# Optimization experiments

Measured on AMD Instinct MI355X. Metric: run time of the kernel, lower is better.

## Reference

```python
import jax, jax.numpy as jnp
import numpy as np

B, S, D = 2, 256, 768
NUM_SPANS = 3
PROJ_DIM = 128


def _span_indices(seq_len):
    # (i, j) pairs exactly as the original double loop enumerates them;
    # span_idx fills slots 0..N-1 of the zero-initialized buffer sequentially.
    si, ei = [], []
    for i in range(seq_len):
        for j in range(i, min(seq_len, i + NUM_SPANS)):
            si.append(i)
            ei.append(j)
    return np.asarray(si, np.int32), np.asarray(ei, np.int32)


def setup_inputs() -> dict:
    key = jax.random.key(0)
    ks = jax.random.split(key, 6)
    sc = 0.02
    return {
        "hidden": jax.random.normal(ks[0], (B, S, D), jnp.float32),
        "width_emb": jax.random.normal(ks[1], (NUM_SPANS, D), jnp.float32) * sc,
        "w_span": jax.random.normal(ks[2], (3 * D, D), jnp.float32) * sc,
        "b_span": jnp.zeros((D,), jnp.float32),
        "w_cls": jax.random.normal(ks[3], (D, 1), jnp.float32) * sc,
        "b_cls": jnp.zeros((1,), jnp.float32),
        "w_p1": jax.random.normal(ks[4], (D, D), jnp.float32) * sc,
        "b_p1": jnp.zeros((D,), jnp.float32),
        "w_p2": jax.random.normal(ks[5], (D, PROJ_DIM), jnp.float32) * sc,
        "b_p2": jnp.zeros((PROJ_DIM,), jnp.float32),
    }


def reference(hidden, width_emb, w_span, b_span, w_cls, b_cls, w_p1, b_p1, w_p2, b_p2):
    Bv, Sv, Dv = hidden.shape
    total = Sv * (Sv + 1) // 2  # size of the zero-padded span buffer
    si, ei = _span_indices(Sv)
    n_valid = si.shape[0]  # 3*S - 3 actually-filled spans

    start = hidden[:, si]                      # [B, N, D] fused gather
    end = hidden[:, ei]                        # [B, N, D]
    w = width_emb[ei - si]                     # [N, D] width-embed lookup
    valid = jnp.concatenate(
        [start, end, jnp.broadcast_to(w[None], (Bv, n_valid, Dv))], axis=-1
    )  # [B, N, 3D]
    pad = jnp.zeros((Bv, total - n_valid, 3 * Dv), hidden.dtype)
    span_vecs = jnp.concatenate([valid, pad], axis=1)  # [B, total, 3D]

    span = span_vecs @ w_span + b_span          # span_rep: [B, total, D]
    logits = (span @ w_cls + b_cls)[..., 0]     # classifier: [B, total]
    proj = jax.nn.relu(span @ w_p1 + b_p1) @ w_p2 + b_p2  # [B, total, 128]
    return logits, proj
```

## Files before the change

kernel.cpp:

```cpp
#include <hip/hip_runtime.h>


typedef unsigned short u16;
typedef __attribute__((ext_vector_type(8))) short bf16x8;
typedef __attribute__((ext_vector_type(8))) unsigned short u16x8;
typedef __attribute__((ext_vector_type(4))) float f32x4;

#define D 768
#define S 256
#define TOTAL 32896
#define NVALID 765
#define NPADROW (TOTAL - NVALID)
#define PD 128
#define LOGITS_SZ (2 * TOTAL)
#define MROWS 1088

#define WS_P1   0
#define WS_TPAD 835584
#define WS_L    836352
#define WS_LW   837376
#define WS_LPAD 837379
#define WS_PPAD 837380
#define US_BYTE_OFF (837632 * 4)
#define US_HH  0
#define US_HL  835584
#define US_AH  1671168
#define US_AL  2064384
#define US_B1H 2457600
#define US_B1L 3637248
#define US_W1H 4816896
#define US_W1L 5406720

__device__ __forceinline__ u16 f2bf(float v) {
    unsigned u = __float_as_uint(v);
    u += 0x7fffu + ((u >> 16) & 1u);
    return (u16)(u >> 16);
}
__device__ __forceinline__ float bf2f(u16 h) {
    return __uint_as_float(((unsigned)h) << 16);
}

__device__ __forceinline__ void span_iw(int k, int& i, int& w) {
    if (k < 762)      { i = k / 3;  w = k - i * 3; }
    else if (k < 764) { i = 254;    w = k - 762; }
    else              { i = 255;    w = 0; }
}

__global__ __launch_bounds__(256) void k_prep(const float* __restrict__ hidden,
                                              const float* __restrict__ width_emb,
                                              const float* __restrict__ w_span,
                                              const float* __restrict__ b_span,
                                              const float* __restrict__ w_cls,
                                              const float* __restrict__ b_cls,
                                              const float* __restrict__ w_p1,
                                              const float* __restrict__ b_p1,
                                              float* __restrict__ ws) {
    u16* us = (u16*)((char*)ws + US_BYTE_OFF);
    const int bid = blockIdx.x, tid = threadIdx.x;
    __shared__ u16 Th[64][72];
    __shared__ u16 Tl[64][72];
    __shared__ float red[256];

    if (bid < 192) {
        const int e0 = bid * 2048 + tid * 8;
        float4 v0 = *(const float4*)&hidden[e0];
        float4 v1 = *(const float4*)&hidden[e0 + 4];
        float f[8] = {v0.x, v0.y, v0.z, v0.w, v1.x, v1.y, v1.z, v1.w};
        u16x8 h, l;
        #pragma unroll
        for (int c = 0; c < 8; ++c) {
            u16 hh = f2bf(f[c]);
            h[c] = hh;
            l[c] = f2bf(f[c] - bf2f(hh));
        }
        *(u16x8*)&us[US_AH + e0] = h;
        *(u16x8*)&us[US_AL + e0] = l;
        return;
    }
    const float* tsrc = nullptr;
    u16 *tdh = nullptr, *tdl = nullptr;
    int kb = 0, nb = 0;
    if (bid < 480) {
        int t2 = bid - 192;
        int g = t2 / 144, rem = t2 % 144;
        kb = rem / 12; nb = rem % 12;
        tsrc = w_span + (size_t)g * D * D;
        tdh = us + US_B1H + (size_t)g * D * D;
        tdl = us + US_B1L + (size_t)g * D * D;
    } else if (bid < 624) {
        int t3 = bid - 480;
        kb = t3 / 12; nb = t3 % 12;
        tsrc = w_p1;
        tdh = us + US_W1H;
        tdl = us + US_W1L;
    }
    if (tsrc) {
        #pragma unroll
        for (int r4 = 0; r4 < 4; ++r4) {
            const int srow = r4 * 16 + (tid >> 4);
            const int scol = (tid & 15) * 4;
            float4 v = *(const float4*)&tsrc[(size_t)(kb * 64 + srow) * D + nb * 64 + scol];
            float f[4] = {v.x, v.y, v.z, v.w};
            #pragma unroll
            for (int c = 0; c < 4; ++c) {
                u16 hh = f2bf(f[c]);
                Th[scol + c][srow] = hh;
                Tl[scol + c][srow] = f2bf(f[c] - bf2f(hh));
            }
        }
        __syncthreads();
        const int orow = tid >> 2, kp = (tid & 3) * 16;
        const size_t didx = (size_t)(nb * 64 + orow) * D + kb * 64 + kp;
        *(u16x8*)&tdh[didx]     = *(const u16x8*)&Th[orow][kp];
        *(u16x8*)&tdh[didx + 8] = *(const u16x8*)&Th[orow][kp + 8];
        *(u16x8*)&tdl[didx]     = *(const u16x8*)&Tl[orow][kp];
        *(u16x8*)&tdl[didx + 8] = *(const u16x8*)&Tl[orow][kp + 8];
        return;
    }
    const int dl = tid & 63, kc = tid >> 6;
    if (bid < 660) {
        const int t4 = bid - 624;
        const int w = t4 / 12, seg = t4 % 12;
        const int d = seg * 64 + dl;
        const float* Aw = w_span + (size_t)(2 * D) * D;
        const float* we = width_emb + w * D;
        float p = 0.f;
        #pragma unroll 4
        for (int k = kc * 192; k < kc * 192 + 192; ++k)
            p = fmaf(we[k], Aw[(size_t)k * D + d], p);
        red[tid] = p; __syncthreads();
        if (kc == 0) {
            float v = red[dl] + red[64 + dl] + red[128 + dl] + red[192 + dl] + b_span[d];
            u16 hh = f2bf(v);
            const size_t idx = (size_t)(1024 + w) * D + d;
            us[US_HH + idx] = hh;
            us[US_HL + idx] = f2bf(v - bf2f(hh));
        }
    } else if (bid < 672) {
        const int d = (bid - 660) * 64 + dl;
        float p = 0.f;
        #pragma unroll 4
        for (int k = kc * 192; k < kc * 192 + 192; ++k)
            p = fmaf(b_span[k], w_p1[(size_t)k * D + d], p);
        red[tid] = p; __syncthreads();
        if (kc == 0) {
            float v = red[dl] + red[64 + dl] + red[128 + dl] + red[192 + dl] + b_p1[d];
            ws[WS_TPAD + d] = fmaxf(v, 0.f);
        }
    } else {
        if (tid < 64) {
            float a = 0.f;
            #pragma unroll
            for (int i = 0; i < 12; ++i) a = fmaf(b_span[tid + 64 * i], w_cls[tid + 64 * i], a);
            for (int off = 32; off > 0; off >>= 1) a += __shfl_down(a, off, 64);
            if (tid == 0) ws[WS_LPAD] = a + b_cls[0];
        }
    }
}

#define MFMA(A, B, C) __builtin_amdgcn_mfma_f32_16x16x32_bf16(A, B, C, 0, 0, 0)

__global__ __launch_bounds__(256) void k_mg1(const float* __restrict__ w_p2,
                                             const float* __restrict__ b_p2,
                                             float* __restrict__ ws) {
    u16* us = (u16*)((char*)ws + US_BYTE_OFF);
    const int bid = blockIdx.x, tid = threadIdx.x;
    __shared__ u16 LA_h[64][40], LA_l[64][40], LB_h[64][40], LB_l[64][40];
    __shared__ float redp[128];
    if (bid < 192) {
        const int mt = bid / 24, nt = bid % 24;
        const int m0 = mt * 64, n0 = nt * 64;
        const int row = tid >> 2, kp = (tid & 3) * 8;
        const u16* Ah = us + US_AH; const u16* Al = us + US_AL;
        const u16* Bh = us + US_B1H; const u16* Bl = us + US_B1L;
        const size_t aoff = (size_t)(m0 + row) * D + kp;
        const size_t boff = (size_t)(n0 + row) * D + kp;
        u16x8 ra_h = *(const u16x8*)&Ah[aoff];
        u16x8 ra_l = *(const u16x8*)&Al[aoff];
        u16x8 rb_h = *(const u16x8*)&Bh[boff];
        u16x8 rb_l = *(const u16x8*)&Bl[boff];
        const int wv = tid >> 6, lane = tid & 63;
        const int wm = wv & 1, wn = wv >> 1;
        const int lr = lane & 15, lk = (lane >> 4) * 8;
        f32x4 acc00 = {0,0,0,0}, acc01 = {0,0,0,0}, acc10 = {0,0,0,0}, acc11 = {0,0,0,0};
        for (int kt = 0; kt < 24; ++kt) {
            *(u16x8*)&LA_h[row][kp] = ra_h;
            *(u16x8*)&LA_l[row][kp] = ra_l;
            *(u16x8*)&LB_h[row][kp] = rb_h;
            *(u16x8*)&LB_l[row][kp] = rb_l;
            __syncthreads();
            if (kt < 23) {
                ra_h = *(const u16x8*)&Ah[aoff + (kt + 1) * 32];
                ra_l = *(const u16x8*)&Al[aoff + (kt + 1) * 32];
                rb_h = *(const u16x8*)&Bh[boff + (kt + 1) * 32];
                rb_l = *(const u16x8*)&Bl[boff + (kt + 1) * 32];
            }
            bf16x8 ah0 = *(const bf16x8*)&LA_h[wm * 32 + lr][lk];
            bf16x8 ah1 = *(const bf16x8*)&LA_h[wm * 32 + 16 + lr][lk];
            bf16x8 al0 = *(const bf16x8*)&LA_l[wm * 32 + lr][lk];
            bf16x8 al1 = *(const bf16x8*)&LA_l[wm * 32 + 16 + lr][lk];
            bf16x8 bh0 = *(const bf16x8*)&LB_h[wn * 32 + lr][lk];
            bf16x8 bh1 = *(const bf16x8*)&LB_h[wn * 32 + 16 + lr][lk];
            bf16x8 bl0 = *(const bf16x8*)&LB_l[wn * 32 + lr][lk];
            bf16x8 bl1 = *(const bf16x8*)&LB_l[wn * 32 + 16 + lr][lk];
            acc00 = MFMA(ah0, bh0, acc00); acc00 = MFMA(ah0, bl0, acc00); acc00 = MFMA(al0, bh0, acc00);
            acc01 = MFMA(ah0, bh1, acc01); acc01 = MFMA(ah0, bl1, acc01); acc01 = MFMA(al0, bh1, acc01);
            acc10 = MFMA(ah1, bh0, acc10); acc10 = MFMA(ah1, bl0, acc10); acc10 = MFMA(al1, bh0, acc10);
            acc11 = MFMA(ah1, bh1, acc11); acc11 = MFMA(ah1, bl1, acc11); acc11 = MFMA(al1, bh1, acc11);
            __syncthreads();
        }
        const int g = (n0 >= D);
        u16* Hh = us + US_HH; u16* Hl = us + US_HL;
        #define WR1(ACC, FM, FN) { \
            const int rr0 = g * 512 + m0 + wm * 32 + FM * 16 + (lane >> 4) * 4; \
            const int cc = n0 - g * D + wn * 32 + FN * 16 + lr; \
            _Pragma("unroll") \
            for (int r = 0; r < 4; ++r) { \
                float v = ACC[r]; \
                u16 hh = f2bf(v); \
                const size_t idx = (size_t)(rr0 + r) * D + cc; \
                Hh[idx] = hh; Hl[idx] = f2bf(v - bf2f(hh)); \
            } }
        WR1(acc00, 0, 0) WR1(acc01, 0, 1) WR1(acc10, 1, 0) WR1(acc11, 1, 1)
        #undef WR1
    } else {
        const int j = tid & 127, h2 = tid >> 7;
        float acc = 0.f;
        #pragma unroll 4
        for (int it = 0; it < 384; ++it) {
            const int d = h2 * 384 + it;
            acc = fmaf(ws[WS_TPAD + d], w_p2[(size_t)d * PD + j], acc);
        }
        if (h2) redp[j] = acc;
        __syncthreads();
        if (!h2) ws[WS_PPAD + j] = acc + redp[j] + b_p2[j];
    }
}

__global__ __launch_bounds__(256) void k_mg2(const float* __restrict__ w_cls,
                                             const float* __restrict__ b_cls,
                                             float* __restrict__ ws) {
    u16* us = (u16*)((char*)ws + US_BYTE_OFF);
    const int bid = blockIdx.x, tid = threadIdx.x;
    __shared__ u16 LA_h[64][40], LA_l[64][40], LB_h[64][40], LB_l[64][40];
    if (bid < 204) {
        const int mt = bid / 12, nt = bid % 12;
        const int m0 = mt * 64, n0 = nt * 64;
        const int row = tid >> 2, kp = (tid & 3) * 8;
        const u16* Ah = us + US_HH; const u16* Al = us + US_HL;
        const u16* Bh = us + US_W1H; const u16* Bl = us + US_W1L;
        const size_t aoff = (size_t)(m0 + row) * D + kp;
        const size_t boff = (size_t)(n0 + row) * D + kp;
        u16x8 ra_h = *(const u16x8*)&Ah[aoff];
        u16x8 ra_l = *(const u16x8*)&Al[aoff];
        u16x8 rb_h = *(const u16x8*)&Bh[boff];
        u16x8 rb_l = *(const u16x8*)&Bl[boff];
        const int wv = tid >> 6, lane = tid & 63;
        const int wm = wv & 1, wn = wv >> 1;
        const int lr = lane & 15, lk = (lane >> 4) * 8;
        f32x4 acc00 = {0,0,0,0}, acc01 = {0,0,0,0}, acc10 = {0,0,0,0}, acc11 = {0,0,0,0};
        for (int kt = 0; kt < 24; ++kt) {
            *(u16x8*)&LA_h[row][kp] = ra_h;
            *(u16x8*)&LA_l[row][kp] = ra_l;
            *(u16x8*)&LB_h[row][kp] = rb_h;
            *(u16x8*)&LB_l[row][kp] = rb_l;
            __syncthreads();
            if (kt < 23) {
                ra_h = *(const u16x8*)&Ah[aoff + (kt + 1) * 32];
                ra_l = *(const u16x8*)&Al[aoff + (kt + 1) * 32];
                rb_h = *(const u16x8*)&Bh[boff + (kt + 1) * 32];
                rb_l = *(const u16x8*)&Bl[boff + (kt + 1) * 32];
            }
            bf16x8 ah0 = *(const bf16x8*)&LA_h[wm * 32 + lr][lk];
            bf16x8 ah1 = *(const bf16x8*)&LA_h[wm * 32 + 16 + lr][lk];
            bf16x8 al0 = *(const bf16x8*)&LA_l[wm * 32 + lr][lk];
            bf16x8 al1 = *(const bf16x8*)&LA_l[wm * 32 + 16 + lr][lk];
            bf16x8 bh0 = *(const bf16x8*)&LB_h[wn * 32 + lr][lk];
            bf16x8 bh1 = *(const bf16x8*)&LB_h[wn * 32 + 16 + lr][lk];
            bf16x8 bl0 = *(const bf16x8*)&LB_l[wn * 32 + lr][lk];
            bf16x8 bl1 = *(const bf16x8*)&LB_l[wn * 32 + 16 + lr][lk];
            acc00 = MFMA(ah0, bh0, acc00); acc00 = MFMA(ah0, bl0, acc00); acc00 = MFMA(al0, bh0, acc00);
            acc01 = MFMA(ah0, bh1, acc01); acc01 = MFMA(ah0, bl1, acc01); acc01 = MFMA(al0, bh1, acc01);
            acc10 = MFMA(ah1, bh0, acc10); acc10 = MFMA(ah1, bl0, acc10); acc10 = MFMA(al1, bh0, acc10);
            acc11 = MFMA(ah1, bh1, acc11); acc11 = MFMA(ah1, bl1, acc11); acc11 = MFMA(al1, bh1, acc11);
            __syncthreads();
        }
        float* P1 = ws + WS_P1;
        #define WR2(ACC, FM, FN) { \
            const int rr0 = m0 + wm * 32 + FM * 16 + (lane >> 4) * 4; \
            const int cc = n0 + wn * 32 + FN * 16 + lr; \
            _Pragma("unroll") \
            for (int r = 0; r < 4; ++r) \
                P1[(size_t)(rr0 + r) * D + cc] = ACC[r]; \
            }
        WR2(acc00, 0, 0) WR2(acc01, 0, 1) WR2(acc10, 1, 0) WR2(acc11, 1, 1)
        #undef WR2
    } else if (bid < 236) {
        const int w64 = tid >> 6, lane = tid & 63;
        const int rbase = (bid - 204) * 32 + w64 * 8;
        for (int rr = 0; rr < 8; ++rr) {
            const int r = rbase + rr;
            const u16* hh = us + US_HH + (size_t)r * D;
            const u16* hl = us + US_HL + (size_t)r * D;
            float a = 0.f;
            #pragma unroll
            for (int i = 0; i < 12; ++i) {
                const int d = lane + 64 * i;
                a = fmaf(bf2f(hh[d]) + bf2f(hl[d]), w_cls[d], a);
            }
            for (int off = 32; off > 0; off >>= 1) a += __shfl_down(a, off, 64);
            if (lane == 0) ws[WS_L + r] = a;
        }
    } else {
        if (tid < 192) {
            const int w = tid >> 6, lane = tid & 63;
            const u16* hh = us + US_HH + (size_t)(1024 + w) * D;
            const u16* hl = us + US_HL + (size_t)(1024 + w) * D;
            float a = 0.f;
            #pragma unroll
            for (int i = 0; i < 12; ++i) {
                const int d = lane + 64 * i;
                a = fmaf(bf2f(hh[d]) + bf2f(hl[d]), w_cls[d], a);
            }
            for (int off = 32; off > 0; off >>= 1) a += __shfl_down(a, off, 64);
            if (lane == 0) ws[WS_LW + w] = a + b_cls[0];
        }
    }
}

__global__ __launch_bounds__(256) void k_stage3(const float* __restrict__ w_p2,
                                                const float* __restrict__ b_p1,
                                                const float* __restrict__ b_p2,
                                                const float* __restrict__ ws,
                                                float* __restrict__ out) {
    const int bid = blockIdx.x, tid = threadIdx.x;
    if (bid < 512) {
        const int t0 = bid * 256 + tid;
        if (t0 < 2 * NPADROW) {
            int b = t0 / NPADROW;
            out[b * TOTAL + NVALID + (t0 - b * NPADROW)] = ws[WS_LPAD];
        }
        const float4 pp = *(const float4*)&ws[WS_PPAD + ((tid & 31) << 2)];
        float4* out4 = (float4*)(out + LOGITS_SZ);
        const long long totalU = (long long)2 * NPADROW * 32;
        for (long long u = t0; u < totalU; u += 131072) {
            int rb = (int)(u >> 5);
            int b = rb / NPADROW;
            int kk = rb - b * NPADROW;
            out4[((size_t)b * TOTAL + NVALID + kk) * 32 + (int)(u & 31)] = pp;
        }
        return;
    }
    const int sb = bid - 512;
    __shared__ float tld[D * 5];
    __shared__ float red[4 * PD];
    const float* P1 = ws + WS_P1;
    {
        const int s = tid >> 6, dl = tid & 63;
        const int q = sb * 4 + s;
        const int v = q < 1530;
        const int qc = v ? q : 0;
        const int b = qc >= 765;
        const int k = qc - 765 * b;
        int i, w; span_iw(k, i, w);
        const size_t rs = (size_t)(b * S + i) * D;
        const size_t re = (size_t)(512 + b * S + i + w) * D;
        const size_t rw = (size_t)(1024 + w) * D;
        #pragma unroll
        for (int p = 0; p < 12; ++p) {
            const int dd = dl + 64 * p;
            float val = P1[rs + dd] + P1[re + dd] + P1[rw + dd] + b_p1[dd];
            tld[dd * 5 + s] = v ? fmaxf(val, 0.f) : 0.f;
        }
    }
    if (tid < 4) {
        int q2 = sb * 4 + tid;
        if (q2 < 1530) {
            int b2 = q2 >= 765, k2 = q2 - 765 * b2, i2, w2;
            span_iw(k2, i2, w2);
            out[b2 * TOTAL + k2] = ws[WS_L + b2 * S + i2]
                                 + ws[WS_L + 512 + b2 * S + i2 + w2] + ws[WS_LW + w2];
        }
    }
    __syncthreads();
    const int j = tid & 127, h = tid >> 7;
    float a[4] = {0.f, 0.f, 0.f, 0.f};
    const float* wp = w_p2 + (size_t)h * 384 * PD + j;
    const float* tb = tld + h * 384 * 5;
    #pragma unroll 4
    for (int it = 0; it < 384; ++it) {
        float wv = wp[(size_t)it * PD];
        #pragma unroll
        for (int s4 = 0; s4 < 4; ++s4)
            a[s4] = fmaf(wv, tb[it * 5 + s4], a[s4]);
    }
    if (h) {
        #pragma unroll
        for (int s4 = 0; s4 < 4; ++s4) red[s4 * PD + j] = a[s4];
    }
    __syncthreads();
    if (!h) {
        const float bp = b_p2[j];
        #pragma unroll
        for (int s4 = 0; s4 < 4; ++s4) {
            int q2 = sb * 4 + s4;
            if (q2 < 1530) {
                int b2 = q2 >= 765, k2 = q2 - 765 * b2;
                out[LOGITS_SZ + ((size_t)b2 * TOTAL + k2) * PD + j] =
                    a[s4] + red[s4 * PD + j] + bp;
            }
        }
    }
}

extern "C" void kernel_launch(void* const* d_in, const int* in_sizes, int n_in,
                              void* d_out, int out_size, void* d_ws, size_t ws_size,
                              hipStream_t stream) {
    const float* hidden    = (const float*)d_in[0];
    const float* width_emb = (const float*)d_in[1];
    const float* w_span    = (const float*)d_in[2];
    const float* b_span    = (const float*)d_in[3];
    const float* w_cls     = (const float*)d_in[4];
    const float* b_cls     = (const float*)d_in[5];
    const float* w_p1      = (const float*)d_in[6];
    const float* b_p1      = (const float*)d_in[7];
    const float* w_p2      = (const float*)d_in[8];
    const float* b_p2      = (const float*)d_in[9];
    float* out = (float*)d_out;
    float* ws  = (float*)d_ws;

    k_prep<<<673, 256, 0, stream>>>(hidden, width_emb, w_span, b_span, w_cls, b_cls,
                                    w_p1, b_p1, ws);
    k_mg1<<<193, 256, 0, stream>>>(w_p2, b_p2, ws);
    k_mg2<<<237, 256, 0, stream>>>(w_cls, b_cls, ws);
    k_stage3<<<895, 256, 0, stream>>>(w_p2, b_p1, b_p2, ws, out);
}
```

Before: 182.7 us.

## Use per-wave LDS-free MFMA tiles and finer span blocks for more parallelism

Both split-bf16 GEMMs drop their 64x64 block tiles that were staged through shared memory and synchronised every k-step. Each wave now loads its own 16x32 tile operands straight from global memory into registers, which gives many more waves and no barriers. The pad-row projection is moved from the first GEMM kernel into the second. The stage-3 kernel now handles 2 spans per block instead of 4, so it launches more blocks. The cost is more redundant global or L2 traffic because tiles are no longer shared through LDS, and each block in stage 3 reuses w_p2 less.

```diff
diff --git a/kernel.cpp b/kernel.cpp
--- a/kernel.cpp
+++ b/kernel.cpp
@@ -159,149 +159,105 @@
 }
 
 #define MFMA(A, B, C) __builtin_amdgcn_mfma_f32_16x16x32_bf16(A, B, C, 0, 0, 0)
-
-__global__ __launch_bounds__(256) void k_mg1(const float* __restrict__ w_p2,
-                                             const float* __restrict__ b_p2,
-                                             float* __restrict__ ws) {
+#define LD8(P) (*(const bf16x8*)(P))
+
+__global__ __launch_bounds__(256) void k_g1(float* __restrict__ ws) {
+    u16* us = (u16*)((char*)ws + US_BYTE_OFF);
+    const int wid = blockIdx.x * 4 + (threadIdx.x >> 6);
+    const int lane = threadIdx.x & 63;
+    const int mt = wid & 31, nt = wid >> 5;
+    const int m0 = mt * 16, n0 = nt * 32;
+    const int lr = lane & 15, lk8 = (lane >> 4) * 8;
+    const u16* Ah = us + US_AH; const u16* Al = us + US_AL;
+    const u16* Bh = us + US_B1H; const u16* Bl = us + US_B1L;
+    const size_t aoff = (size_t)(m0 + lr) * D + lk8;
+    const size_t b0 = (size_t)(n0 + lr) * D + lk8;
+    const size_t b1 = b0 + (size_t)16 * D;
+    f32x4 acc0 = {0,0,0,0}, acc1 = {0,0,0,0};
+    bf16x8 ah = LD8(Ah + aoff), al = LD8(Al + aoff);
+    bf16x8 bh0 = LD8(Bh + b0), bl0 = LD8(Bl + b0);
+    bf16x8 bh1 = LD8(Bh + b1), bl1 = LD8(Bl + b1);
+    for (int kt = 0; kt < 24; ++kt) {
+        bf16x8 cah = ah, cal = al, cbh0 = bh0, cbl0 = bl0, cbh1 = bh1, cbl1 = bl1;
+        if (kt < 23) {
+            const size_t o = (size_t)(kt + 1) * 32;
+            ah = LD8(Ah + aoff + o); al = LD8(Al + aoff + o);
+            bh0 = LD8(Bh + b0 + o);  bl0 = LD8(Bl + b0 + o);
+            bh1 = LD8(Bh + b1 + o);  bl1 = LD8(Bl + b1 + o);
+        }
+        acc0 = MFMA(cah, cbh0, acc0);
+        acc0 = MFMA(cah, cbl0, acc0);
+        acc0 = MFMA(cal, cbh0, acc0);
+        acc1 = MFMA(cah, cbh1, acc1);
+        acc1 = MFMA(cah, cbl1, acc1);
+        acc1 = MFMA(cal, cbh1, acc1);
+    }
+    const int g = (n0 >= D);
+    const int cb = n0 - g * D;
+    const int row0 = g * 512 + m0 + (lane >> 4) * 4;
+    u16* Hh = us + US_HH; u16* Hl = us + US_HL;
+    #pragma unroll
+    for (int r = 0; r < 4; ++r) {
+        const size_t base = (size_t)(row0 + r) * D;
+        float v0 = acc0[r], v1 = acc1[r];
+        u16 h0 = f2bf(v0), h1 = f2bf(v1);
+        Hh[base + cb + lr] = h0;       Hl[base + cb + lr] = f2bf(v0 - bf2f(h0));
+        Hh[base + cb + 16 + lr] = h1;  Hl[base + cb + 16 + lr] = f2bf(v1 - bf2f(h1));
+    }
+}
+
+__global__ __launch_bounds__(256) void k_g2(const float* __restrict__ w_cls,
+                                            const float* __restrict__ b_cls,
+                                            const float* __restrict__ w_p2,
+                                            const float* __restrict__ b_p2,
+                                            float* __restrict__ ws) {
     u16* us = (u16*)((char*)ws + US_BYTE_OFF);
     const int bid = blockIdx.x, tid = threadIdx.x;
-    __shared__ u16 LA_h[64][40], LA_l[64][40], LB_h[64][40], LB_l[64][40];
-    __shared__ float redp[128];
-    if (bid < 192) {
-        const int mt = bid / 24, nt = bid % 24;
-        const int m0 = mt * 64, n0 = nt * 64;
-        const int row = tid >> 2, kp = (tid & 3) * 8;
-        const u16* Ah = us + US_AH; const u16* Al = us + US_AL;
-        const u16* Bh = us + US_B1H; const u16* Bl = us + US_B1L;
-        const size_t aoff = (size_t)(m0 + row) * D + kp;
-        const size_t boff = (size_t)(n0 + row) * D + kp;
-        u16x8 ra_h = *(const u16x8*)&Ah[aoff];
-        u16x8 ra_l = *(const u16x8*)&Al[aoff];
-        u16x8 rb_h = *(const u16x8*)&Bh[boff];
-        u16x8 rb_l = *(const u16x8*)&Bl[boff];
-        const int wv = tid >> 6, lane = tid & 63;
-        const int wm = wv & 1, wn = wv >> 1;
-        const int lr = lane & 15, lk = (lane >> 4) * 8;
-        f32x4 acc00 = {0,0,0,0}, acc01 = {0,0,0,0}, acc10 = {0,0,0,0}, acc11 = {0,0,0,0};
+    const u16* Hh = us + US_HH; const u16* Hl = us + US_HL;
+    if (bid < 390) {
+        const int wid = bid * 4 + (tid >> 6);
+        const int lane = tid & 63;
+        const int mt = wid % 65, nt = wid / 65;
+        const int m0 = mt * 16, n0 = nt * 32;
+        const int lr = lane & 15, lk8 = (lane >> 4) * 8;
+        const u16* Bh = us + US_W1H; const u16* Bl = us + US_W1L;
+        const size_t aoff = (size_t)(m0 + lr) * D + lk8;
+        const size_t b0 = (size_t)(n0 + lr) * D + lk8;
+        const size_t b1 = b0 + (size_t)16 * D;
+        f32x4 acc0 = {0,0,0,0}, acc1 = {0,0,0,0};
+        bf16x8 ah = LD8(Hh + aoff), al = LD8(Hl + aoff);
+        bf16x8 bh0 = LD8(Bh + b0), bl0 = LD8(Bl + b0);
+        bf16x8 bh1 = LD8(Bh + b1), bl1 = LD8(Bl + b1);
         for (int kt = 0; kt < 24; ++kt) {
-            *(u16x8*)&LA_h[row][kp] = ra_h;
-            *(u16x8*)&LA_l[row][kp] = ra_l;
-            *(u16x8*)&LB_h[row][kp] = rb_h;
-            *(u16x8*)&LB_l[row][kp] = rb_l;
-            __syncthreads();
+            bf16x8 cah = ah, cal = al, cbh0 = bh0, cbl0 = bl0, cbh1 = bh1, cbl1 = bl1;
             if (kt < 23) {
-                ra_h = *(const u16x8*)&Ah[aoff + (kt + 1) * 32];
-                ra_l = *(const u16x8*)&Al[aoff + (kt + 1) * 32];
-                rb_h = *(const u16x8*)&Bh[boff + (kt + 1) * 32];
-                rb_l = *(const u16x8*)&Bl[boff + (kt + 1) * 32];
+                const size_t o = (size_t)(kt + 1) * 32;
+                ah = LD8(Hh + aoff + o); al = LD8(Hl + aoff + o);
+                bh0 = LD8(Bh + b0 + o);  bl0 = LD8(Bl + b0 + o);
+                bh1 = LD8(Bh + b1 + o);  bl1 = LD8(Bl + b1 + o);
             }
-            bf16x8 ah0 = *(const bf16x8*)&LA_h[wm * 32 + lr][lk];
-            bf16x8 ah1 = *(const bf16x8*)&LA_h[wm * 32 + 16 + lr][lk];
-            bf16x8 al0 = *(const bf16x8*)&LA_l[wm * 32 + lr][lk];
-            bf16x8 al1 = *(const bf16x8*)&LA_l[wm * 32 + 16 + lr][lk];
-            bf16x8 bh0 = *(const bf16x8*)&LB_h[wn * 32 + lr][lk];
-            bf16x8 bh1 = *(const bf16x8*)&LB_h[wn * 32 + 16 + lr][lk];
-            bf16x8 bl0 = *(const bf16x8*)&LB_l[wn * 32 + lr][lk];
-            bf16x8 bl1 = *(const bf16x8*)&LB_l[wn * 32 + 16 + lr][lk];
-            acc00 = MFMA(ah0, bh0, acc00); acc00 = MFMA(ah0, bl0, acc00); acc00 = MFMA(al0, bh0, acc00);
-            acc01 = MFMA(ah0, bh1, acc01); acc01 = MFMA(ah0, bl1, acc01); acc01 = MFMA(al0, bh1, acc01);
-            acc10 = MFMA(ah1, bh0, acc10); acc10 = MFMA(ah1, bl0, acc10); acc10 = MFMA(al1, bh0, acc10);
-            acc11 = MFMA(ah1, bh1, acc11); acc11 = MFMA(ah1, bl1, acc11); acc11 = MFMA(al1, bh1, acc11);
-            __syncthreads();
-        }
-        const int g = (n0 >= D);
-        u16* Hh = us + US_HH; u16* Hl = us + US_HL;
-        #define WR1(ACC, FM, FN) { \
-            const int rr0 = g * 512 + m0 + wm * 32 + FM * 16 + (lane >> 4) * 4; \
-            const int cc = n0 - g * D + wn * 32 + FN * 16 + lr; \
-            _Pragma("unroll") \
-            for (int r = 0; r < 4; ++r) { \
-                float v = ACC[r]; \
-                u16 hh = f2bf(v); \
-                const size_t idx = (size_t)(rr0 + r) * D + cc; \
-                Hh[idx] = hh; Hl[idx] = f2bf(v - bf2f(hh)); \
-            } }
-        WR1(acc00, 0, 0) WR1(acc01, 0, 1) WR1(acc10, 1, 0) WR1(acc11, 1, 1)
-        #undef WR1
-    } else {
-        const int j = tid & 127, h2 = tid >> 7;
-        float acc = 0.f;
-        #pragma unroll 4
-        for (int it = 0; it < 384; ++it) {
-            const int d = h2 * 384 + it;
-            acc = fmaf(ws[WS_TPAD + d], w_p2[(size_t)d * PD + j], acc);
-        }
-        if (h2) redp[j] = acc;
-        __syncthreads();
-        if (!h2) ws[WS_PPAD + j] = acc + redp[j] + b_p2[j];
-    }
-}
-
-__global__ __launch_bounds__(256) void k_mg2(const float* __restrict__ w_cls,
-                                             const float* __restrict__ b_cls,
-                                             float* __restrict__ ws) {
-    u16* us = (u16*)((char*)ws + US_BYTE_OFF);
-    const int bid = blockIdx.x, tid = threadIdx.x;
-    __shared__ u16 LA_h[64][40], LA_l[64][40], LB_h[64][40], LB_l[64][40];
-    if (bid < 204) {
-        const int mt = bid / 12, nt = bid % 12;
-        const int m0 = mt * 64, n0 = nt * 64;
-        const int row = tid >> 2, kp = (tid & 3) * 8;
-        const u16* Ah = us + US_HH; const u16* Al = us + US_HL;
-        const u16* Bh = us + US_W1H; const u16* Bl = us + US_W1L;
-        const size_t aoff = (size_t)(m0 + row) * D + kp;
-        const size_t boff = (size_t)(n0 + row) * D + kp;
-        u16x8 ra_h = *(const u16x8*)&Ah[aoff];
-        u16x8 ra_l = *(const u16x8*)&Al[aoff];
-        u16x8 rb_h = *(const u16x8*)&Bh[boff];
-        u16x8 rb_l = *(const u16x8*)&Bl[boff];
-        const int wv = tid >> 6, lane = tid & 63;
-        const int wm = wv & 1, wn = wv >> 1;
-        const int lr = lane & 15, lk = (lane >> 4) * 8;
-        f32x4 acc00 = {0,0,0,0}, acc01 = {0,0,0,0}, acc10 = {0,0,0,0}, acc11 = {0,0,0,0};
-        for (int kt = 0; kt < 24; ++kt) {
-            *(u16x8*)&LA_h[row][kp] = ra_h;
-            *(u16x8*)&LA_l[row][kp] = ra_l;
-            *(u16x8*)&LB_h[row][kp] = rb_h;
-            *(u16x8*)&LB_l[row][kp] = rb_l;
-            __syncthreads();
-            if (kt < 23) {
-                ra_h = *(const u16x8*)&Ah[aoff + (kt + 1) * 32];
-                ra_l = *(const u16x8*)&Al[aoff + (kt + 1) * 32];
-                rb_h = *(const u16x8*)&Bh[boff + (kt + 1) * 32];
-                rb_l = *(const u16x8*)&Bl[boff + (kt + 1) * 32];
-            }
-            bf16x8 ah0 = *(const bf16x8*)&LA_h[wm * 32 + lr][lk];
-            bf16x8 ah1 = *(const bf16x8*)&LA_h[wm * 32 + 16 + lr][lk];
-            bf16x8 al0 = *(const bf16x8*)&LA_l[wm * 32 + lr][lk];
-            bf16x8 al1 = *(const bf16x8*)&LA_l[wm * 32 + 16 + lr][lk];
-            bf16x8 bh0 = *(const bf16x8*)&LB_h[wn * 32 + lr][lk];
-            bf16x8 bh1 = *(const bf16x8*)&LB_h[wn * 32 + 16 + lr][lk];
-            bf16x8 bl0 = *(const bf16x8*)&LB_l[wn * 32 + lr][lk];
-            bf16x8 bl1 = *(const bf16x8*)&LB_l[wn * 32 + 16 + lr][lk];
-            acc00 = MFMA(ah0, bh0, acc00); acc00 = MFMA(ah0, bl0, acc00); acc00 = MFMA(al0, bh0, acc00);
-            acc01 = MFMA(ah0, bh1, acc01); acc01 = MFMA(ah0, bl1, acc01); acc01 = MFMA(al0, bh1, acc01);
-            acc10 = MFMA(ah1, bh0, acc10); acc10 = MFMA(ah1, bl0, acc10); acc10 = MFMA(al1, bh0, acc10);
-            acc11 = MFMA(ah1, bh1, acc11); acc11 = MFMA(ah1, bl1, acc11); acc11 = MFMA(al1, bh1, acc11);
-            __syncthreads();
+            acc0 = MFMA(cah, cbh0, acc0);
+            acc0 = MFMA(cah, cbl0, acc0);
+            acc0 = MFMA(cal, cbh0, acc0);
+            acc1 = MFMA(cah, cbh1, acc1);
+            acc1 = MFMA(cah, cbl1, acc1);
+            acc1 = MFMA(cal, cbh1, acc1);
         }
         float* P1 = ws + WS_P1;
-        #define WR2(ACC, FM, FN) { \
-            const int rr0 = m0 + wm * 32 + FM * 16 + (lane >> 4) * 4; \
-            const int cc = n0 + wn * 32 + FN * 16 + lr; \
-            _Pragma("unroll") \
-            for (int r = 0; r < 4; ++r) \
-                P1[(size_t)(rr0 + r) * D + cc] = ACC[r]; \
-            }
-        WR2(acc00, 0, 0) WR2(acc01, 0, 1) WR2(acc10, 1, 0) WR2(acc11, 1, 1)
-        #undef WR2
-    } else if (bid < 236) {
+        const int row0 = m0 + (lane >> 4) * 4;
+        #pragma unroll
+        for (int r = 0; r < 4; ++r) {
+            const size_t base = (size_t)(row0 + r) * D;
+            P1[base + n0 + lr] = acc0[r];
+            P1[base + n0 + 16 + lr] = acc1[r];
+        }
+    } else if (bid < 422) {
         const int w64 = tid >> 6, lane = tid & 63;
-        const int rbase = (bid - 204) * 32 + w64 * 8;
+        const int rbase = (bid - 390) * 32 + w64 * 8;
         for (int rr = 0; rr < 8; ++rr) {
             const int r = rbase + rr;
-            const u16* hh = us + US_HH + (size_t)r * D;
-            const u16* hl = us + US_HL + (size_t)r * D;
+            const u16* hh = Hh + (size_t)r * D;
+            const u16* hl = Hl + (size_t)r * D;
             float a = 0.f;
             #pragma unroll
             for (int i = 0; i < 12; ++i) {
@@ -311,11 +267,11 @@
             for (int off = 32; off > 0; off >>= 1) a += __shfl_down(a, off, 64);
             if (lane == 0) ws[WS_L + r] = a;
         }
-    } else {
+    } else if (bid == 422) {
         if (tid < 192) {
             const int w = tid >> 6, lane = tid & 63;
-            const u16* hh = us + US_HH + (size_t)(1024 + w) * D;
-            const u16* hl = us + US_HL + (size_t)(1024 + w) * D;
+            const u16* hh = Hh + (size_t)(1024 + w) * D;
+            const u16* hl = Hl + (size_t)(1024 + w) * D;
             float a = 0.f;
             #pragma unroll
             for (int i = 0; i < 12; ++i) {
@@ -325,6 +281,18 @@
             for (int off = 32; off > 0; off >>= 1) a += __shfl_down(a, off, 64);
             if (lane == 0) ws[WS_LW + w] = a + b_cls[0];
         }
+    } else {
+        __shared__ float redp[128];
+        const int j = tid & 127, h2 = tid >> 7;
+        float acc = 0.f;
+        #pragma unroll 4
+        for (int it = 0; it < 384; ++it) {
+            const int d = h2 * 384 + it;
+            acc = fmaf(ws[WS_TPAD + d], w_p2[(size_t)d * PD + j], acc);
+        }
+        if (h2) redp[j] = acc;
+        __syncthreads();
+        if (!h2) ws[WS_PPAD + j] = acc + redp[j] + b_p2[j];
     }
 }
 
@@ -352,63 +320,53 @@
         return;
     }
     const int sb = bid - 512;
-    __shared__ float tld[D * 5];
-    __shared__ float red[4 * PD];
+    __shared__ float tld[D * 2];
+    __shared__ float red[2 * PD];
     const float* P1 = ws + WS_P1;
     {
-        const int s = tid >> 6, dl = tid & 63;
-        const int q = sb * 4 + s;
-        const int v = q < 1530;
-        const int qc = v ? q : 0;
-        const int b = qc >= 765;
-        const int k = qc - 765 * b;
+        const int s = tid >> 7, dl = tid & 127;
+        const int q = sb * 2 + s;
+        const int b = q >= 765;
+        const int k = q - 765 * b;
         int i, w; span_iw(k, i, w);
         const size_t rs = (size_t)(b * S + i) * D;
         const size_t re = (size_t)(512 + b * S + i + w) * D;
         const size_t rw = (size_t)(1024 + w) * D;
         #pragma unroll
-        for (int p = 0; p < 12; ++p) {
-            const int dd = dl + 64 * p;
+        for (int p = 0; p < 6; ++p) {
+            const int dd = dl + 128 * p;
             float val = P1[rs + dd] + P1[re + dd] + P1[rw + dd] + b_p1[dd];
-            tld[dd * 5 + s] = v ? fmaxf(val, 0.f) : 0.f;
-        }
-    }
-    if (tid < 4) {
-        int q2 = sb * 4 + tid;
-        if (q2 < 1530) {
-            int b2 = q2 >= 765, k2 = q2 - 765 * b2, i2, w2;
-            span_iw(k2, i2, w2);
-            out[b2 * TOTAL + k2] = ws[WS_L + b2 * S + i2]
-                                 + ws[WS_L + 512 + b2 * S + i2 + w2] + ws[WS_LW + w2];
-        }
+            tld[dd * 2 + s] = fmaxf(val, 0.f);
+        }
+    }
+    if (tid < 2) {
+        const int q2 = sb * 2 + tid;
+        const int b2 = q2 >= 765, k2 = q2 - 765 * b2;
+        int i2, w2; span_iw(k2, i2, w2);
+        out[b2 * TOTAL + k2] = ws[WS_L + b2 * S + i2]
+                             + ws[WS_L + 512 + b2 * S + i2 + w2] + ws[WS_LW + w2];
     }
     __syncthreads();
     const int j = tid & 127, h = tid >> 7;
-    float a[4] = {0.f, 0.f, 0.f, 0.f};
+    float a0 = 0.f, a1 = 0.f;
     const float* wp = w_p2 + (size_t)h * 384 * PD + j;
-    const float* tb = tld + h * 384 * 5;
+    const float* tb = tld + h * 384 * 2;
     #pragma unroll 4
     for (int it = 0; it < 384; ++it) {
-        float wv = wp[(size_t)it * PD];
-        #pragma unroll
-        for (int s4 = 0; s4 < 4; ++s4)
-            a[s4] = fmaf(wv, tb[it * 5 + s4], a[s4]);
-    }
-    if (h) {
-        #pragma unroll
-        for (int s4 = 0; s4 < 4; ++s4) red[s4 * PD + j] = a[s4];
-    }
+        const float wv = wp[(size_t)it * PD];
+        a0 = fmaf(wv, tb[it * 2], a0);
+        a1 = fmaf(wv, tb[it * 2 + 1], a1);
+    }
+    if (h) { red[j] = a0; red[PD + j] = a1; }
     __syncthreads();
     if (!h) {
         const float bp = b_p2[j];
-        #pragma unroll
-        for (int s4 = 0; s4 < 4; ++s4) {
-            int q2 = sb * 4 + s4;
-            if (q2 < 1530) {
-                int b2 = q2 >= 765, k2 = q2 - 765 * b2;
-                out[LOGITS_SZ + ((size_t)b2 * TOTAL + k2) * PD + j] =
-                    a[s4] + red[s4 * PD + j] + bp;
-            }
+        const float v[2] = {a0 + red[j] + bp, a1 + red[PD + j] + bp};
+        #pragma unroll
+        for (int s4 = 0; s4 < 2; ++s4) {
+            const int q2 = sb * 2 + s4;
+            const int b2 = q2 >= 765, k2 = q2 - 765 * b2;
+            out[LOGITS_SZ + ((size_t)b2 * TOTAL + k2) * PD + j] = v[s4];
         }
     }
 }
@@ -431,7 +389,7 @@
 
     k_prep<<<673, 256, 0, stream>>>(hidden, width_emb, w_span, b_span, w_cls, b_cls,
                                     w_p1, b_p1, ws);
-    k_mg1<<<193, 256, 0, stream>>>(w_p2, b_p2, ws);
-    k_mg2<<<237, 256, 0, stream>>>(w_cls, b_cls, ws);
-    k_stage3<<<895, 256, 0, stream>>>(w_p2, b_p1, b_p2, ws, out);
-}
+    k_g1<<<384, 256, 0, stream>>>(ws);
+    k_g2<<<424, 256, 0, stream>>>(w_cls, b_cls, w_p2, b_p2, ws);
+    k_stage3<<<1277, 256, 0, stream>>>(w_p2, b_p1, b_p2, ws, out);
+}
```

New measurement: 202.4 us. +10.7%, slower.
